# Performance work log

Hardware: AMD Instinct MI355X
Metric: run time of the kernel (lower is better)

The kernel has to match this reference:

```python
import jax, jax.numpy as jnp
import numpy as np

KSIZE = 3          # self.ksize
SCALE = 10.0       # self.softmax_scale
EPS = 1e-4         # escape_NaN, added per-element before the reduce_sum
MASK_DS = 8        # int_fs[3] != 32 -> mask downsampled by 8*rate


def extract_patches(x, k, s):
    """torch extract_image_patches with 'same' padding.
    x: [B,C,H,W] -> [B, L, C, k, k] with L = out_h*out_w (row-major positions),
    matching unfold -> view(B,C,k,k,L) -> permute(0,4,1,2,3)."""
    B, C, H, W = x.shape
    oh, ow = -(-H // s), -(-W // s)
    pr = max(0, (oh - 1) * s + k - H)
    pc = max(0, (ow - 1) * s + k - W)
    pt, pl = pr // 2, pc // 2
    xp = jnp.pad(x, ((0, 0), (0, 0), (pt, pr - pt), (pl, pc - pl)))
    sl = [xp[:, :, i:i + (oh - 1) * s + 1:s, j:j + (ow - 1) * s + 1:s]
          for i in range(k) for j in range(k)]          # k*k static slices
    p = jnp.stack(sl, axis=2).reshape(B, C, k, k, oh, ow)
    return p.transpose(0, 4, 5, 1, 2, 3).reshape(B, oh * ow, C, k, k)


def contextual_attention_score(f, b, mask):
    # rate=1 -> both F.interpolate(scale_factor=1.0) calls are identity.
    B, C, Hf, Wf = f.shape
    Hb, Wb = b.shape[2], b.shape[3]
    # background patches used as correlation filters: [B, Lb, C, 3, 3]
    w = extract_patches(b, KSIZE, 1)
    # mask: nearest downsample by 8 == strided subsampling
    mask_s = mask[:, :, ::MASK_DS, ::MASK_DS]
    m = extract_patches(mask_s, KSIZE, 1)[0]            # [Lb, 1, 3, 3] (batch 0 only, as in source)
    pm = jnp.mean(jax.lax.stop_gradient(m), axis=(1, 2, 3))
    mm = (pm == 0.0).astype(f.dtype).reshape(1, -1, 1, 1)  # [1, Lb, 1, 1]
    # L2-normalize each filter (EPS added per element before the sum, as in source)
    denom = jnp.sqrt(jnp.sum(w * w + EPS, axis=(2, 3, 4), keepdims=True))
    wn = w / denom
    # per-sample conv2d(xi_padded, wi_normed) == patch cross-correlation:
    fp = extract_patches(f, KSIZE, 1)                   # [B, Lf, C, 3, 3]
    y = jnp.einsum('bqckl,bpckl->bpq', fp, wn)          # [B, Lb, Lf]
    y = y.reshape(B, Hb * Wb, Hf, Wf) * mm
    y = jax.nn.softmax(y * SCALE, axis=1) * mm
    return y                                            # module returns `score`


def setup_inputs():
    key = jax.random.key(0)
    k1, k2 = jax.random.split(key)
    f = jax.random.normal(k1, (4, 128, 64, 64), dtype=jnp.float32)
    b = jax.random.normal(k2, (4, 128, 64, 64), dtype=jnp.float32)
    # binary inpainting mask at image resolution (1 = hole / unavailable)
    mask = jnp.zeros((4, 1, 512, 512), dtype=jnp.float32)
    mask = mask.at[:, :, 192:320, 192:320].set(1.0)
    return {"f": f, "b": b, "mask": mask}


def reference(f, b, mask):
    return contextual_attention_score(f, b, mask)
```

## Files before the change

kernel.cpp:

```cpp
#include <hip/hip_runtime.h>
#include <hip/hip_bf16.h>
#include <math.h>


typedef float f32x4 __attribute__((ext_vector_type(4)));
typedef short bf16x8 __attribute__((ext_vector_type(8)));

#define NB 4
#define NC 128
#define NP 4096ull
#define LOG2E_SCALE 14.426950408889634f
#define EPS_TERM (1152.0f * 1e-4f)

#define SZ_S      (4ull * NP * NP * 4ull)
#define SZ_BT     (4ull * NP * NC * 2ull)
#define OFF_S     0ull
#define OFF_BT_HI (OFF_S + SZ_S)
#define OFF_BT_LO (OFF_BT_HI + SZ_BT)
#define OFF_FT_HI (OFF_BT_LO + SZ_BT)
#define OFF_FT_LO (OFF_FT_HI + SZ_BT)
#define OFF_NORM2 (OFF_FT_LO + SZ_BT)
#define OFF_COEF  (OFF_NORM2 + 4ull * NP * 4ull)
#define OFF_MM    (OFF_COEF + 4ull * NP * 4ull)
#define OFF_PART  (OFF_MM + NP * 4ull)
#define OFF_LINV  (OFF_PART + 4ull * 16ull * NP * 4ull)

__global__ __launch_bounds__(256) void k_norm2(const float* __restrict__ bin,
                                               float* __restrict__ norm2) {
    int idx = blockIdx.x * 256 + threadIdx.x;
    int b = idx >> 12, u = idx & 4095;
    const float* src = bin + (size_t)b * NC * NP + u;
    float s = 0.f;
#pragma unroll 8
    for (int c = 0; c < NC; ++c) { float x = src[(size_t)c * NP]; s += x * x; }
    norm2[idx] = s;
}

__global__ __launch_bounds__(256) void k_coef(const float* __restrict__ norm2,
                                              const float* __restrict__ mask,
                                              float* __restrict__ coef,
                                              float* __restrict__ mmArr) {
    int idx = blockIdx.x * 256 + threadIdx.x;
    int b = idx >> 12, p = idx & 4095;
    int ph = p >> 6, pw = p & 63;
    float ns = 0.f, ms = 0.f;
#pragma unroll
    for (int dy = -1; dy <= 1; ++dy)
#pragma unroll
        for (int dx = -1; dx <= 1; ++dx) {
            int hh = ph + dy, ww = pw + dx;
            if ((unsigned)hh < 64u && (unsigned)ww < 64u) {
                ns += norm2[b * 4096 + hh * 64 + ww];
                ms += mask[(size_t)(hh * 512 + ww) * 8];
            }
        }
    float mmv = (ms == 0.f) ? 1.f : 0.f;
    coef[idx] = mmv * LOG2E_SCALE / sqrtf(ns + EPS_TERM);
    if (b == 0) mmArr[p] = mmv;
}

__global__ __launch_bounds__(256) void k_convert(const float* __restrict__ fin,
                                                 const float* __restrict__ bin,
                                                 __bf16* __restrict__ bt_hi, __bf16* __restrict__ bt_lo,
                                                 __bf16* __restrict__ ft_hi, __bf16* __restrict__ ft_lo) {
    __shared__ float tile[64][65];
    int u0 = blockIdx.x * 64;
    int k0 = blockIdx.y * 64;
    int z = blockIdx.z;
    int arr = z & 1, b = z >> 1;
    const float* src = (arr ? fin : bin) + (size_t)b * NC * NP;
    __bf16* dhi = (arr ? ft_hi : bt_hi) + (size_t)b * NP * NC;
    __bf16* dlo = (arr ? ft_lo : bt_lo) + (size_t)b * NP * NC;
    int t = threadIdx.x;
#pragma unroll
    for (int i = 0; i < 16; ++i) {
        int lin = i * 256 + t;
        int kl = lin >> 6, ul = lin & 63;
        tile[kl][ul] = src[(size_t)(k0 + kl) * NP + u0 + ul];
    }
    __syncthreads();
#pragma unroll
    for (int i = 0; i < 16; ++i) {
        int lin = i * 256 + t;
        int ul = lin >> 6, kl = lin & 63;
        float x = tile[kl][ul];
        __bf16 h = (__bf16)x;
        float hf = (float)h;
        __bf16 l = (__bf16)(x - hf);
        size_t o = (size_t)(u0 + ul) * NC + (k0 + kl);
        dhi[o] = h; dlo[o] = l;
    }
}

__global__ __launch_bounds__(256) void k_matmul(const __bf16* __restrict__ bt_hi,
                                                const __bf16* __restrict__ bt_lo,
                                                const __bf16* __restrict__ ft_hi,
                                                const __bf16* __restrict__ ft_lo,
                                                float* __restrict__ S) {
    int t = threadIdx.x;
    int lane = t & 63;
    int w = t >> 6;
    int b = blockIdx.z;
    int m_base = blockIdx.y * 128 + (w >> 1) * 64;
    int n_base = blockIdx.x * 128 + (w & 1) * 64;
    int l15 = lane & 15;
    int quad = lane >> 4;
    size_t bo = (size_t)b * NP * NC;
    const __bf16* Ah = bt_hi + bo;
    const __bf16* Al = bt_lo + bo;
    const __bf16* Bh = ft_hi + bo;
    const __bf16* Bl = ft_lo + bo;

    f32x4 acc[4][4];
#pragma unroll
    for (int i = 0; i < 4; ++i)
#pragma unroll
        for (int j = 0; j < 4; ++j) acc[i][j] = (f32x4){0.f, 0.f, 0.f, 0.f};

#pragma unroll
    for (int ks = 0; ks < 4; ++ks) {
        int k = ks * 32 + quad * 8;
        bf16x8 ah[4], al[4], bh[4], bl[4];
#pragma unroll
        for (int mt = 0; mt < 4; ++mt) {
            size_t o = (size_t)(m_base + mt * 16 + l15) * NC + k;
            ah[mt] = *(const bf16x8*)(Ah + o);
            al[mt] = *(const bf16x8*)(Al + o);
        }
#pragma unroll
        for (int nt = 0; nt < 4; ++nt) {
            size_t o = (size_t)(n_base + nt * 16 + l15) * NC + k;
            bh[nt] = *(const bf16x8*)(Bh + o);
            bl[nt] = *(const bf16x8*)(Bl + o);
        }
#pragma unroll
        for (int mt = 0; mt < 4; ++mt)
#pragma unroll
            for (int nt = 0; nt < 4; ++nt) {
                acc[mt][nt] = __builtin_amdgcn_mfma_f32_16x16x32_bf16(ah[mt], bh[nt], acc[mt][nt], 0, 0, 0);
                acc[mt][nt] = __builtin_amdgcn_mfma_f32_16x16x32_bf16(ah[mt], bl[nt], acc[mt][nt], 0, 0, 0);
                acc[mt][nt] = __builtin_amdgcn_mfma_f32_16x16x32_bf16(al[mt], bh[nt], acc[mt][nt], 0, 0, 0);
            }
    }
    float* Sb = S + (size_t)b * NP * NP;
#pragma unroll
    for (int mt = 0; mt < 4; ++mt)
#pragma unroll
        for (int nt = 0; nt < 4; ++nt) {
            int col = n_base + nt * 16 + l15;
            int row0 = m_base + mt * 16 + quad * 4;
#pragma unroll
            for (int r = 0; r < 4; ++r)
                Sb[(size_t)(row0 + r) * NP + col] = acc[mt][nt][r];
        }
}

__global__ __launch_bounds__(256) void k_scores(const float* __restrict__ S,
                                                const float* __restrict__ coef,
                                                float* __restrict__ out,
                                                float* __restrict__ part) {
    int t = threadIdx.x;
    int b = blockIdx.z;
    int pc = blockIdx.y;
    int q = blockIdx.x * 256 + t;
    int qh = q >> 6, qw = q & 63;
    const float* Sb = S + (size_t)b * NP * NP;
    float* outb = out + (size_t)b * NP * NP;
    const float* cf = coef + b * 4096;
    float acc = 0.f;
    for (int pi = 0; pi < 256; ++pi) {
        int p = pc * 256 + pi;
        int ph = p >> 6, pw = p & 63;
        const float* Sp = Sb + (size_t)p * NP + q;
        float y = 0.f;
#pragma unroll
        for (int dy = -1; dy <= 1; ++dy) {
            bool okh = ((unsigned)(ph + dy) < 64u) & ((unsigned)(qh + dy) < 64u);
#pragma unroll
            for (int dx = -1; dx <= 1; ++dx) {
                bool ok = okh & ((unsigned)(pw + dx) < 64u) & ((unsigned)(qw + dx) < 64u);
                int s = dy * 64 + dx;
                float v = ok ? Sp[(ptrdiff_t)s * 4097] : 0.f;
                y += v;
            }
        }
        float e = exp2f(cf[p] * y);
        outb[(size_t)p * NP + q] = e;
        acc += e;
    }
    part[(size_t)(b * 16 + pc) * NP + q] = acc;
}

__global__ __launch_bounds__(256) void k_rsum(const float* __restrict__ part,
                                              float* __restrict__ linv) {
    int idx = blockIdx.x * 256 + threadIdx.x;
    int b = idx >> 12, q = idx & 4095;
    float s = 0.f;
#pragma unroll
    for (int pc = 0; pc < 16; ++pc) s += part[(size_t)(b * 16 + pc) * NP + q];
    linv[idx] = 1.0f / s;
}

__global__ __launch_bounds__(256) void k_fixup(float* __restrict__ out,
                                               const float* __restrict__ mmArr,
                                               const float* __restrict__ linv) {
    int bp = blockIdx.x;
    int b = bp >> 12, p = bp & 4095;
    float mv = mmArr[p];
    float* row = out + (size_t)bp * NP;
    const float* lv = linv + b * 4096;
    int t = threadIdx.x;
#pragma unroll
    for (int it = 0; it < 4; ++it) {
        int q = it * 1024 + t * 4;
        f32x4 v = *(f32x4*)(row + q);
        f32x4 L = *(const f32x4*)(lv + q);
        v.x *= mv * L.x; v.y *= mv * L.y; v.z *= mv * L.z; v.w *= mv * L.w;
        *(f32x4*)(row + q) = v;
    }
}

extern "C" void kernel_launch(void* const* d_in, const int* in_sizes, int n_in,
                              void* d_out, int out_size, void* d_ws, size_t ws_size,
                              hipStream_t stream) {
    (void)in_sizes; (void)n_in; (void)out_size; (void)ws_size;
    const float* f_in = (const float*)d_in[0];
    const float* b_in = (const float*)d_in[1];
    const float* mask = (const float*)d_in[2];
    float* out = (float*)d_out;
    char* ws = (char*)d_ws;

    float*  S     = (float*)(ws + OFF_S);
    __bf16* bt_hi = (__bf16*)(ws + OFF_BT_HI);
    __bf16* bt_lo = (__bf16*)(ws + OFF_BT_LO);
    __bf16* ft_hi = (__bf16*)(ws + OFF_FT_HI);
    __bf16* ft_lo = (__bf16*)(ws + OFF_FT_LO);
    float*  norm2 = (float*)(ws + OFF_NORM2);
    float*  coef  = (float*)(ws + OFF_COEF);
    float*  mmArr = (float*)(ws + OFF_MM);
    float*  part  = (float*)(ws + OFF_PART);
    float*  linv  = (float*)(ws + OFF_LINV);

    k_norm2  <<<64, 256, 0, stream>>>(b_in, norm2);
    k_coef   <<<64, 256, 0, stream>>>(norm2, mask, coef, mmArr);
    k_convert<<<dim3(64, 2, 8), 256, 0, stream>>>(f_in, b_in, bt_hi, bt_lo, ft_hi, ft_lo);
    k_matmul <<<dim3(32, 32, 4), 256, 0, stream>>>(bt_hi, bt_lo, ft_hi, ft_lo, S);
    k_scores <<<dim3(16, 16, 4), 256, 0, stream>>>(S, coef, out, part);
    k_rsum   <<<64, 256, 0, stream>>>(part, linv);
    k_fixup  <<<16384, 256, 0, stream>>>(out, mmArr, linv);
}
```

Measured before the change: 870.3 us.

## Split score pass into sum-exp and recompute-write passes, vectorize stencil

Replaces the exp-write-then-normalize scheme with two passes over S. The first computes only the per-column exp sums, and the second recomputes the stencil and exp and writes the final normalized, masked output directly. This removes the extra read-modify-write of the 256MB output, at the cost of a second stencil read of S and duplicated exp work. The stencil loads are vectorized to four columns per thread with edge masking, and the grid uses more, smaller p-chunks (with a larger partial-sum buffer).

Measured after the change: 758.8 us. 1.15x faster.

```diff
diff --git a/kernel.cpp b/kernel.cpp
--- a/kernel.cpp
+++ b/kernel.cpp
@@ -14,8 +14,8 @@
 
 #define SZ_S      (4ull * NP * NP * 4ull)
 #define SZ_BT     (4ull * NP * NC * 2ull)
-#define OFF_S     0ull
-#define OFF_BT_HI (OFF_S + SZ_S)
+#define OFF_S     1024ull
+#define OFF_BT_HI (OFF_S + SZ_S + 1024ull)
 #define OFF_BT_LO (OFF_BT_HI + SZ_BT)
 #define OFF_FT_HI (OFF_BT_LO + SZ_BT)
 #define OFF_FT_LO (OFF_FT_HI + SZ_BT)
@@ -23,7 +23,7 @@
 #define OFF_COEF  (OFF_NORM2 + 4ull * NP * 4ull)
 #define OFF_MM    (OFF_COEF + 4ull * NP * 4ull)
 #define OFF_PART  (OFF_MM + NP * 4ull)
-#define OFF_LINV  (OFF_PART + 4ull * 16ull * NP * 4ull)
+#define OFF_LINV  (OFF_PART + 4ull * 128ull * NP * 4ull)
 
 __global__ __launch_bounds__(256) void k_norm2(const float* __restrict__ bin,
                                                float* __restrict__ norm2) {
@@ -155,40 +155,50 @@
         }
 }
 
-__global__ __launch_bounds__(256) void k_scores(const float* __restrict__ S,
+__device__ __forceinline__ f32x4 stencil9(const float* __restrict__ rowbase,
+                                          int ph, int pw, int qh, int qw0) {
+    f32x4 y = {0.f, 0.f, 0.f, 0.f};
+#pragma unroll
+    for (int dy = -1; dy <= 1; ++dy) {
+        bool okh = ((unsigned)(ph + dy) < 64u) & ((unsigned)(qh + dy) < 64u);
+#pragma unroll
+        for (int dx = -1; dx <= 1; ++dx) {
+            bool ok = okh & ((unsigned)(pw + dx) < 64u);
+            const int s = dy * 64 + dx;
+            ptrdiff_t off = ok ? (ptrdiff_t)s * 4097 : 0;
+            f32x4 t = *(const f32x4*)(rowbase + off);
+            if (!ok) t = (f32x4){0.f, 0.f, 0.f, 0.f};
+            if (dx == -1 && qw0 == 0)  t.x = 0.f;
+            if (dx == 1  && qw0 == 60) t.w = 0.f;
+            y += t;
+        }
+    }
+    return y;
+}
+
+__global__ __launch_bounds__(256) void k_sumexp(const float* __restrict__ S,
                                                 const float* __restrict__ coef,
-                                                float* __restrict__ out,
                                                 float* __restrict__ part) {
     int t = threadIdx.x;
     int b = blockIdx.z;
     int pc = blockIdx.y;
-    int q = blockIdx.x * 256 + t;
-    int qh = q >> 6, qw = q & 63;
+    int q0 = blockIdx.x * 1024 + t * 4;
+    int qh = q0 >> 6, qw0 = q0 & 63;
     const float* Sb = S + (size_t)b * NP * NP;
-    float* outb = out + (size_t)b * NP * NP;
-    const float* cf = coef + b * 4096;
-    float acc = 0.f;
-    for (int pi = 0; pi < 256; ++pi) {
-        int p = pc * 256 + pi;
+    const float* cf = coef + (b << 12);
+    f32x4 acc = {0.f, 0.f, 0.f, 0.f};
+    for (int pi = 0; pi < 32; ++pi) {
+        int p = pc * 32 + pi;
         int ph = p >> 6, pw = p & 63;
-        const float* Sp = Sb + (size_t)p * NP + q;
-        float y = 0.f;
-#pragma unroll
-        for (int dy = -1; dy <= 1; ++dy) {
-            bool okh = ((unsigned)(ph + dy) < 64u) & ((unsigned)(qh + dy) < 64u);
-#pragma unroll
-            for (int dx = -1; dx <= 1; ++dx) {
-                bool ok = okh & ((unsigned)(pw + dx) < 64u) & ((unsigned)(qw + dx) < 64u);
-                int s = dy * 64 + dx;
-                float v = ok ? Sp[(ptrdiff_t)s * 4097] : 0.f;
-                y += v;
-            }
-        }
-        float e = exp2f(cf[p] * y);
-        outb[(size_t)p * NP + q] = e;
-        acc += e;
-    }
-    part[(size_t)(b * 16 + pc) * NP + q] = acc;
+        const float* rowbase = Sb + (size_t)p * NP + q0;
+        f32x4 y = stencil9(rowbase, ph, pw, qh, qw0);
+        float c = cf[p];
+        acc.x += exp2f(c * y.x);
+        acc.y += exp2f(c * y.y);
+        acc.z += exp2f(c * y.z);
+        acc.w += exp2f(c * y.w);
+    }
+    *(f32x4*)(part + ((size_t)(b * 128 + pc) << 12) + q0) = acc;
 }
 
 __global__ __launch_bounds__(256) void k_rsum(const float* __restrict__ part,
@@ -196,27 +206,37 @@
     int idx = blockIdx.x * 256 + threadIdx.x;
     int b = idx >> 12, q = idx & 4095;
     float s = 0.f;
-#pragma unroll
-    for (int pc = 0; pc < 16; ++pc) s += part[(size_t)(b * 16 + pc) * NP + q];
+    for (int pc = 0; pc < 128; ++pc) s += part[((size_t)(b * 128 + pc) << 12) + q];
     linv[idx] = 1.0f / s;
 }
 
-__global__ __launch_bounds__(256) void k_fixup(float* __restrict__ out,
+__global__ __launch_bounds__(256) void k_write(const float* __restrict__ S,
+                                               const float* __restrict__ coef,
                                                const float* __restrict__ mmArr,
-                                               const float* __restrict__ linv) {
-    int bp = blockIdx.x;
-    int b = bp >> 12, p = bp & 4095;
-    float mv = mmArr[p];
-    float* row = out + (size_t)bp * NP;
-    const float* lv = linv + b * 4096;
-    int t = threadIdx.x;
-#pragma unroll
-    for (int it = 0; it < 4; ++it) {
-        int q = it * 1024 + t * 4;
-        f32x4 v = *(f32x4*)(row + q);
-        f32x4 L = *(const f32x4*)(lv + q);
-        v.x *= mv * L.x; v.y *= mv * L.y; v.z *= mv * L.z; v.w *= mv * L.w;
-        *(f32x4*)(row + q) = v;
+                                               const float* __restrict__ linv,
+                                               float* __restrict__ out) {
+    int t = threadIdx.x;
+    int b = blockIdx.z;
+    int pc = blockIdx.y;
+    int q0 = blockIdx.x * 1024 + t * 4;
+    int qh = q0 >> 6, qw0 = q0 & 63;
+    const float* Sb = S + (size_t)b * NP * NP;
+    float* outb = out + (size_t)b * NP * NP;
+    const float* cf = coef + (b << 12);
+    f32x4 L = *(const f32x4*)(linv + (b << 12) + q0);
+    for (int pi = 0; pi < 32; ++pi) {
+        int p = pc * 32 + pi;
+        int ph = p >> 6, pw = p & 63;
+        const float* rowbase = Sb + (size_t)p * NP + q0;
+        f32x4 y = stencil9(rowbase, ph, pw, qh, qw0);
+        float c = cf[p];
+        float mv = mmArr[p];
+        f32x4 o;
+        o.x = exp2f(c * y.x) * mv * L.x;
+        o.y = exp2f(c * y.y) * mv * L.y;
+        o.z = exp2f(c * y.z) * mv * L.z;
+        o.w = exp2f(c * y.w) * mv * L.w;
+        *(f32x4*)(outb + (size_t)p * NP + q0) = o;
     }
 }
 
@@ -245,7 +265,7 @@
     k_coef   <<<64, 256, 0, stream>>>(norm2, mask, coef, mmArr);
     k_convert<<<dim3(64, 2, 8), 256, 0, stream>>>(f_in, b_in, bt_hi, bt_lo, ft_hi, ft_lo);
     k_matmul <<<dim3(32, 32, 4), 256, 0, stream>>>(bt_hi, bt_lo, ft_hi, ft_lo, S);
-    k_scores <<<dim3(16, 16, 4), 256, 0, stream>>>(S, coef, out, part);
+    k_sumexp <<<dim3(4, 128, 4), 256, 0, stream>>>(S, coef, part);
     k_rsum   <<<64, 256, 0, stream>>>(part, linv);
-    k_fixup  <<<16384, 256, 0, stream>>>(out, mmArr, linv);
-}
+    k_write  <<<dim3(4, 128, 4), 256, 0, stream>>>(S, coef, mmArr, linv, out);
+}
```
